# Kernel optimization log

Hardware: AMD Instinct MI355X
Metric: run time of the kernel (lower is better)

The kernel has to match this reference:

```python
import jax, jax.numpy as jnp
import numpy as np

V, H, B, S, T = 512, 1024, 128, 256, 128


def setup_inputs() -> dict:
    key = jax.random.key(0)
    ks = jax.random.split(key, 16)
    s = 1.0 / np.sqrt(H)
    f32 = jnp.float32
    return {
        "encoder_outputs": jax.random.normal(ks[0], (B, S, H), f32),
        "encoder_hidden": jax.random.normal(ks[1], (1, B, H), f32),
        "encoder_cell": jax.random.normal(ks[2], (1, B, H), f32),
        "target_tensor": jax.random.randint(ks[3], (B, T), 0, V),
        "max_length": T,
        "emb": (jax.random.normal(ks[4], (V, H), f32) * s),
        "Wa_w": jax.random.normal(ks[5], (H, H), f32) * s,
        "Wa_b": jnp.zeros((H,), f32),
        "Ua_w": jax.random.normal(ks[6], (H, H), f32) * s,
        "Ua_b": jnp.zeros((H,), f32),
        "Va_w": jax.random.normal(ks[7], (1, H), f32) * s,
        "Va_b": jnp.zeros((1,), f32),
        "W_ih": jax.random.normal(ks[8], (4 * H, 2 * H), f32) * s,
        "W_hh": jax.random.normal(ks[9], (4 * H, H), f32) * s,
        "b_ih": jnp.zeros((4 * H,), f32),
        "b_hh": jnp.zeros((4 * H,), f32),
        "out_w": jax.random.normal(ks[10], (V, H), f32) * s,
        "out_b": jnp.zeros((V,), f32),
    }


def reference(encoder_outputs, encoder_hidden, encoder_cell, target_tensor, max_length,
              emb, Wa_w, Wa_b, Ua_w, Ua_b, Va_w, Va_b,
              W_ih, W_hh, b_ih, b_hh, out_w, out_b):
    # Teacher forcing: decoder input at step i is SOS (=0) then target[:, i-1].
    bsz = encoder_outputs.shape[0]
    sos = jnp.zeros((bsz, 1), dtype=target_tensor.dtype)
    tokens = jnp.concatenate([sos, target_tensor[:, : max_length - 1]], axis=1)  # [B, T]
    xs = emb[tokens].transpose(1, 0, 2)  # [T, B, H] (dropout = identity, eval mode)

    # Ua(keys) is loop-invariant (original recomputes it each step; same math).
    keys_proj = jnp.einsum('bsh,kh->bsk', encoder_outputs, Ua_w) + Ua_b  # [B, S, H]

    def step(carry, emb_t):
        h, c = carry  # [B, H] each
        q = h @ Wa_w.T + Wa_b  # Bahdanau query projection [B, H]
        e = jnp.tanh(q[:, None, :] + keys_proj) @ Va_w[0] + Va_b[0]  # [B, S]
        w = jax.nn.softmax(e, axis=-1)
        ctx = jnp.einsum('bs,bsh->bh', w, encoder_outputs)
        x = jnp.concatenate([emb_t, ctx], axis=-1)  # [B, 2H]
        gates = x @ W_ih.T + b_ih + h @ W_hh.T + b_hh  # [B, 4H], torch order i,f,g,o
        i, f, g, o = jnp.split(gates, 4, axis=-1)
        c_new = jax.nn.sigmoid(f) * c + jax.nn.sigmoid(i) * jnp.tanh(g)
        h_new = jax.nn.sigmoid(o) * jnp.tanh(c_new)
        logits = h_new @ out_w.T + out_b  # [B, V]
        return (h_new, c_new), (logits, w)

    init = (encoder_hidden[0], encoder_cell[0])
    (h_fin, c_fin), (logits, attn) = jax.lax.scan(step, init, xs)
    log_probs = jax.nn.log_softmax(logits.transpose(1, 0, 2), axis=-1)  # [B, T, V]
    return log_probs, h_fin[None], attn.transpose(1, 0, 2)  # hidden [1,B,H], attn [B,T,S]
```

## Files before the change

kernel.cpp:

```cpp
#include <hip/hip_runtime.h>

#define B_ 128
#define S_ 256
#define H_ 1024
#define V_ 512
#define T_ 128
#define G4 4096

typedef __attribute__((ext_vector_type(8))) short bf16x8;
typedef __attribute__((ext_vector_type(4))) float f32x4;

__device__ __forceinline__ float bf2f(unsigned short x) {
    unsigned int u = ((unsigned int)x) << 16;
    return __builtin_bit_cast(float, u);
}
__device__ __forceinline__ unsigned short f2b(float f) {
    unsigned int u = __builtin_bit_cast(unsigned int, f);
    u = u + 0x7fffu + ((u >> 16) & 1u);
    return (unsigned short)(u >> 16);
}
__device__ __forceinline__ float ftanh(float x) {
    float e = __expf(2.f * x);
    return 1.f - 2.f * __builtin_amdgcn_rcpf(e + 1.f);
}
__device__ __forceinline__ float fsigm(float x) {
    return __builtin_amdgcn_rcpf(1.f + __expf(-x));
}
__device__ __forceinline__ void gll16(const void* g, void* l) {
    __builtin_amdgcn_global_load_lds(
        (const __attribute__((address_space(1))) unsigned int*)g,
        (__attribute__((address_space(3))) unsigned int*)l, 16, 0, 0);
}

__global__ void f32_to_bf16_x4(const float4* __restrict__ in, ushort4* __restrict__ out, int n4) {
    int i = blockIdx.x * 256 + threadIdx.x;
    if (i < n4) {
        float4 v = in[i];
        ushort4 o;
        o.x = f2b(v.x); o.y = f2b(v.y); o.z = f2b(v.z); o.w = f2b(v.w);
        out[i] = o;
    }
}

__global__ void cvt_gather(const float* __restrict__ src, int src_ld, int coff,
                           unsigned short* __restrict__ dst, int perm) {
    int i = blockIdx.x * 256 + threadIdx.x;
    int r = i >> 8;
    int c = (i & 255) * 4;
    int sr = perm ? (((r & 3) << 10) + (r >> 2)) : r;
    float4 v = *reinterpret_cast<const float4*>(src + (size_t)sr * src_ld + coff + c);
    ushort4 o;
    o.x = f2b(v.x); o.y = f2b(v.y); o.z = f2b(v.z); o.w = f2b(v.w);
    *reinterpret_cast<ushort4*>(dst + (size_t)r * 1024 + c) = o;
}

__global__ void build_toks(const int* __restrict__ target, int* __restrict__ toks) {
    int idx = blockIdx.x * 256 + threadIdx.x;
    if (idx < T_ * B_) {
        int t = idx / B_, b = idx % B_;
        toks[idx] = (t == 0) ? 0 : target[b * T_ + t - 1];
    }
}

__global__ void build_bsum(const float* __restrict__ b_ih, const float* __restrict__ b_hh,
                           float* __restrict__ bsum) {
    int j = blockIdx.x * 256 + threadIdx.x;
    if (j < G4) {
        int pj = ((j & 3) << 10) + (j >> 2);
        bsum[j] = b_ih[pj] + b_hh[pj];
    }
}

template<int MODE>
__global__ __launch_bounds__(256) void gemm_mf(
    const unsigned short* __restrict__ A,
    const unsigned short* __restrict__ Bw,
    int K, int ldb, int ldc,
    float* __restrict__ C, unsigned short* __restrict__ Cb,
    const float* __restrict__ bias)
{
    __shared__ unsigned short As[2 * 8192];
    __shared__ unsigned short Bs[2 * 8192];
    const int tid = threadIdx.x;
    const int lane = tid & 63;
    const int wv = tid >> 6;
    const int m0 = blockIdx.x * 64;
    const int n0 = blockIdx.y * 64;

    const unsigned short* ga[4];
    const unsigned short* gb[4];
    #pragma unroll
    for (int j = 0; j < 4; ++j) {
        int ci = tid + 256 * j;
        int row = ci >> 4;
        int src = (ci & 15) ^ (row & 7);
        ga[j] = A + (size_t)(m0 + row) * K + src * 8;
        gb[j] = Bw + (size_t)(n0 + row) * ldb + src * 8;
    }

    f32x4 acc[2][2] = {};
    const int r0 = (wv >> 1) * 32;
    const int cq0 = (wv & 1) * 32;
    const int fr = lane & 15;
    const int kg = lane >> 4;

    auto stage = [&](int k0, int p) {
        #pragma unroll
        for (int j = 0; j < 4; ++j) {
            gll16(ga[j] + k0, As + p * 8192 + j * 2048 + wv * 512);
            gll16(gb[j] + k0, Bs + p * 8192 + j * 2048 + wv * 512);
        }
    };

    stage(0, 0);
    stage(128, 1);
    int p = 0;
    for (int k0 = 0; k0 < K; k0 += 128) {
        if (k0 + 128 < K) {
            asm volatile("s_waitcnt vmcnt(8)" ::: "memory");
        } else {
            asm volatile("s_waitcnt vmcnt(0)" ::: "memory");
        }
        __builtin_amdgcn_sched_barrier(0);
        __builtin_amdgcn_s_barrier();
        __builtin_amdgcn_sched_barrier(0);
        const unsigned short* Ab = As + p * 8192;
        const unsigned short* Bb = Bs + p * 8192;
        bf16x8 af[2][4], bfr[2][4];
        #pragma unroll
        for (int f = 0; f < 2; ++f)
            #pragma unroll
            for (int kh = 0; kh < 4; ++kh) {
                int ra = r0 + f * 16 + fr;
                af[f][kh] = *(const bf16x8*)&Ab[ra * 128 + (((kh * 4 + kg) ^ (ra & 7)) << 3)];
                int rb = cq0 + f * 16 + fr;
                bfr[f][kh] = *(const bf16x8*)&Bb[rb * 128 + (((kh * 4 + kg) ^ (rb & 7)) << 3)];
            }
        asm volatile("s_waitcnt lgkmcnt(0)" ::: "memory");
        __builtin_amdgcn_sched_barrier(0);
        __builtin_amdgcn_s_barrier();
        __builtin_amdgcn_sched_barrier(0);
        if (k0 + 256 < K) stage(k0 + 256, p);
        #pragma unroll
        for (int f = 0; f < 2; ++f)
            #pragma unroll
            for (int g = 0; g < 2; ++g)
                #pragma unroll
                for (int kh = 0; kh < 4; ++kh)
                    acc[f][g] = __builtin_amdgcn_mfma_f32_16x16x32_bf16(
                        af[f][kh], bfr[g][kh], acc[f][g], 0, 0, 0);
        p ^= 1;
    }

    const int erow = (lane >> 4) * 4;
    const int ecol = lane & 15;
    #pragma unroll
    for (int f = 0; f < 2; ++f) {
        #pragma unroll
        for (int g = 0; g < 2; ++g) {
            #pragma unroll
            for (int r = 0; r < 4; ++r) {
                int row = m0 + r0 + f * 16 + erow + r;
                int col = n0 + cq0 + g * 16 + ecol;
                float v = acc[f][g][r] + bias[col];
                if (MODE == 0) C[(size_t)row * ldc + col] = v;
                else Cb[(size_t)row * ldc + col] = f2b(v);
            }
        }
    }
}

template<int MODE>
__global__ __launch_bounds__(256) void gemm_n32(
    const unsigned short* __restrict__ A,
    const unsigned short* __restrict__ Bw,
    int K, int ldb, int ldc,
    float* __restrict__ C, unsigned short* __restrict__ Cb,
    const float* __restrict__ bias,
    const float* __restrict__ Pemb,
    const int* __restrict__ toks,
    float* __restrict__ Cq,
    float* __restrict__ Lg,
    const float* __restrict__ bias2,
    int flag)
{
    __shared__ unsigned short As[2 * 8192];
    __shared__ unsigned short Bs[2 * 4096];
    const int tid = threadIdx.x;
    const int lane = tid & 63;
    const int wv = tid >> 6;
    const int m0 = blockIdx.x * 64;
    const int n0 = blockIdx.y * 32;

    const unsigned short* ga[4];
    const unsigned short* gb[2];
    #pragma unroll
    for (int j = 0; j < 4; ++j) {
        int ci = tid + 256 * j;
        int row = ci >> 4;
        int src = (ci & 15) ^ (row & 7);
        ga[j] = A + (size_t)(m0 + row) * K + src * 8;
    }
    #pragma unroll
    for (int j = 0; j < 2; ++j) {
        int ci = tid + 256 * j;
        int row = ci >> 4;
        int src = (ci & 15) ^ (row & 7);
        gb[j] = Bw + (size_t)(n0 + row) * ldb + src * 8;
    }

    f32x4 acc[2] = {};
    const int r0 = (wv >> 1) * 32;
    const int c0 = (wv & 1) * 16;
    const int fr = lane & 15;
    const int kg = lane >> 4;

    auto stage = [&](int k0, int p) {
        #pragma unroll
        for (int j = 0; j < 4; ++j)
            gll16(ga[j] + k0, As + p * 8192 + j * 2048 + wv * 512);
        #pragma unroll
        for (int j = 0; j < 2; ++j)
            gll16(gb[j] + k0, Bs + p * 4096 + j * 2048 + wv * 512);
    };

    stage(0, 0);
    stage(128, 1);
    int p = 0;
    for (int k0 = 0; k0 < K; k0 += 128) {
        if (k0 + 128 < K) {
            asm volatile("s_waitcnt vmcnt(6)" ::: "memory");
        } else {
            asm volatile("s_waitcnt vmcnt(0)" ::: "memory");
        }
        __builtin_amdgcn_sched_barrier(0);
        __builtin_amdgcn_s_barrier();
        __builtin_amdgcn_sched_barrier(0);
        const unsigned short* Ab = As + p * 8192;
        const unsigned short* Bb = Bs + p * 4096;
        bf16x8 af[2][4], bfr[4];
        #pragma unroll
        for (int kh = 0; kh < 4; ++kh) {
            #pragma unroll
            for (int f = 0; f < 2; ++f) {
                int ra = r0 + f * 16 + fr;
                af[f][kh] = *(const bf16x8*)&Ab[ra * 128 + (((kh * 4 + kg) ^ (ra & 7)) << 3)];
            }
            int rb = c0 + fr;
            bfr[kh] = *(const bf16x8*)&Bb[rb * 128 + (((kh * 4 + kg) ^ (rb & 7)) << 3)];
        }
        asm volatile("s_waitcnt lgkmcnt(0)" ::: "memory");
        __builtin_amdgcn_sched_barrier(0);
        __builtin_amdgcn_s_barrier();
        __builtin_amdgcn_sched_barrier(0);
        if (k0 + 256 < K) stage(k0 + 256, p);
        #pragma unroll
        for (int f = 0; f < 2; ++f)
            #pragma unroll
            for (int kh = 0; kh < 4; ++kh)
                acc[f] = __builtin_amdgcn_mfma_f32_16x16x32_bf16(
                    af[f][kh], bfr[kh], acc[f], 0, 0, 0);
        p ^= 1;
    }

    const int erow = (lane >> 4) * 4;
    const int ecol = lane & 15;

    if constexpr (MODE == 4) {
        __shared__ float Lt[64 * 32];
        __syncthreads();
        #pragma unroll
        for (int f = 0; f < 2; ++f)
            #pragma unroll
            for (int r = 0; r < 4; ++r)
                Lt[(r0 + f * 16 + erow + r) * 32 + c0 + ecol] = acc[f][r];
        __syncthreads();
        #pragma unroll
        for (int i = 0; i < 2; ++i) {
            int pi = tid + 256 * i;
            int r = pi >> 3, u = pi & 7;
            int b = m0 + r;
            int hh = (n0 >> 2) + u;
            f32x4 gv = *reinterpret_cast<const f32x4*>(&Lt[r * 32 + u * 4]);
            const float* gp = C + (size_t)b * G4 + n0 + u * 4;
            float iv = gv[0] + gp[0];
            float fv = gv[1] + gp[1];
            float gg = gv[2] + gp[2];
            float ov = gv[3] + gp[3];
            int ci = b * H_ + hh;
            float cn = fsigm(fv) * Cq[ci] + fsigm(iv) * ftanh(gg);
            float hn = fsigm(ov) * ftanh(cn);
            Cq[ci] = cn;
            Cb[ci] = f2b(hn);
            if (flag) Lg[ci] = hn;
        }
    } else {
        #pragma unroll
        for (int f = 0; f < 2; ++f) {
            #pragma unroll
            for (int r = 0; r < 4; ++r) {
                int row = m0 + r0 + f * 16 + erow + r;
                int col = n0 + c0 + ecol;
                float v = acc[f][r];
                if (MODE == 0) {
                    C[(size_t)row * ldc + col] = v + bias[col];
                } else {
                    if (col < H_) {
                        Cq[(size_t)row * H_ + col] = v + bias[col];
                    } else if (col < 5120) {
                        int cg = col - H_;
                        C[(size_t)row * G4 + cg] = v + Pemb[(size_t)toks[row] * G4 + cg];
                    } else {
                        int cl = col - 5120;
                        Lg[(size_t)row * V_ + cl] = v + bias2[cl];
                    }
                }
            }
        }
    }
}

__global__ __launch_bounds__(256) void attn_e(
    const unsigned short* __restrict__ kp,
    const float* __restrict__ q,
    const float* __restrict__ Va,
    const unsigned short* __restrict__ encb,
    float* __restrict__ es_g,
    float* __restrict__ pctx,
    const float* __restrict__ lg,
    float* __restrict__ lp,
    int t)
{
    const int b = blockIdx.x;
    const int sh = blockIdx.y;
    const int tid = threadIdx.x;
    const int lane = tid & 63;
    const int wv = tid >> 6;
    __shared__ float qs[H_];
    __shared__ float vas[H_];
    __shared__ float es[16], pe[16];
    __shared__ float redm[4], reds[4];

    *reinterpret_cast<float4*>(&qs[tid * 4]) =
        *reinterpret_cast<const float4*>(&q[(size_t)b * H_ + tid * 4]);
    *reinterpret_cast<float4*>(&vas[tid * 4]) =
        *reinterpret_cast<const float4*>(&Va[tid * 4]);

    const bool doL = (t > 0) && (sh == 0);
    float a0 = doL ? lg[(size_t)b * V_ + tid] : -3.4e38f;
    float a1 = doL ? lg[(size_t)b * V_ + 256 + tid] : -3.4e38f;
    float mx = fmaxf(a0, a1);
    #pragma unroll
    for (int off = 32; off; off >>= 1) mx = fmaxf(mx, __shfl_xor(mx, off));
    if (lane == 0) redm[wv] = mx;
    __syncthreads();
    mx = fmaxf(fmaxf(redm[0], redm[1]), fmaxf(redm[2], redm[3]));
    float sm = doL ? (__expf(a0 - mx) + __expf(a1 - mx)) : 0.f;
    #pragma unroll
    for (int off = 32; off; off >>= 1) sm += __shfl_xor(sm, off);
    if (lane == 0) reds[wv] = sm;
    __syncthreads();
    if (doL) {
        sm = reds[0] + reds[1] + reds[2] + reds[3];
        float lse = mx + __logf(sm);
        size_t off = ((size_t)b * T_ + (t - 1)) * V_;
        lp[off + tid] = a0 - lse;
        lp[off + tid + 256] = a1 - lse;
    }

    #pragma unroll
    for (int si = 0; si < 4; ++si) {
        int s_loc = wv * 4 + si;
        const unsigned short* kr = kp + (size_t)(b * S_ + sh * 16 + s_loc) * H_;
        float acc = 0.f;
        #pragma unroll
        for (int it = 0; it < 4; ++it) {
            int h4 = lane * 4 + it * 256;
            ushort4 u = *reinterpret_cast<const ushort4*>(kr + h4);
            acc += vas[h4 + 0] * ftanh(qs[h4 + 0] + bf2f(u.x));
            acc += vas[h4 + 1] * ftanh(qs[h4 + 1] + bf2f(u.y));
            acc += vas[h4 + 2] * ftanh(qs[h4 + 2] + bf2f(u.z));
            acc += vas[h4 + 3] * ftanh(qs[h4 + 3] + bf2f(u.w));
        }
        #pragma unroll
        for (int off = 32; off; off >>= 1) acc += __shfl_down(acc, off);
        if (lane == 0) {
            es[s_loc] = acc;
            es_g[(size_t)b * S_ + sh * 16 + s_loc] = acc;
        }
    }
    __syncthreads();

    float mb = es[0];
    #pragma unroll
    for (int i = 1; i < 16; ++i) mb = fmaxf(mb, es[i]);
    if (tid < 16) pe[tid] = __expf(es[tid] - mb);
    __syncthreads();
    const int c0 = tid * 4;
    float ax = 0.f, ay = 0.f, az = 0.f, aw = 0.f;
    #pragma unroll
    for (int sl = 0; sl < 16; ++sl) {
        ushort4 u = *reinterpret_cast<const ushort4*>(
            &encb[(size_t)(b * S_ + sh * 16 + sl) * H_ + c0]);
        float w = pe[sl];
        ax += w * bf2f(u.x);
        ay += w * bf2f(u.y);
        az += w * bf2f(u.z);
        aw += w * bf2f(u.w);
    }
    float4 o4; o4.x = ax; o4.y = ay; o4.z = az; o4.w = aw;
    *reinterpret_cast<float4*>(&pctx[((size_t)b * 16 + sh) * H_ + c0]) = o4;
}

__global__ __launch_bounds__(256) void attn_comb(
    const float* __restrict__ es_g,
    const float* __restrict__ pctx,
    unsigned short* __restrict__ ctxb,
    float* __restrict__ attnOut,
    int t)
{
    const int b = blockIdx.x;
    const int tid = threadIdx.x;
    const int lane = tid & 63;
    const int wv = tid >> 6;
    __shared__ float es[S_], sc[16];
    __shared__ float redm[4], reds[4];

    float x = es_g[(size_t)b * S_ + tid];
    es[tid] = x;
    float mx = x;
    #pragma unroll
    for (int off = 32; off; off >>= 1) mx = fmaxf(mx, __shfl_xor(mx, off));
    if (lane == 0) redm[wv] = mx;
    __syncthreads();
    mx = fmaxf(fmaxf(redm[0], redm[1]), fmaxf(redm[2], redm[3]));
    float ex = __expf(x - mx);
    float sm = ex;
    #pragma unroll
    for (int off = 32; off; off >>= 1) sm += __shfl_xor(sm, off);
    if (lane == 0) reds[wv] = sm;
    __syncthreads();
    sm = reds[0] + reds[1] + reds[2] + reds[3];
    float rZ = __builtin_amdgcn_rcpf(sm);
    attnOut[((size_t)(b * T_ + t)) * S_ + tid] = ex * rZ;
    if (tid < 16) {
        float mb = es[tid * 16];
        #pragma unroll
        for (int j = 1; j < 16; ++j) mb = fmaxf(mb, es[tid * 16 + j]);
        sc[tid] = __expf(mb - mx);
    }
    __syncthreads();
    const int c0 = tid * 4;
    float ax = 0.f, ay = 0.f, az = 0.f, aw = 0.f;
    #pragma unroll
    for (int blk = 0; blk < 16; ++blk) {
        float4 pv = *reinterpret_cast<const float4*>(
            &pctx[((size_t)b * 16 + blk) * H_ + c0]);
        float s = sc[blk];
        ax += s * pv.x; ay += s * pv.y; az += s * pv.z; aw += s * pv.w;
    }
    ushort4 o;
    o.x = f2b(ax * rZ); o.y = f2b(ay * rZ); o.z = f2b(az * rZ); o.w = f2b(aw * rZ);
    *reinterpret_cast<ushort4*>(&ctxb[(size_t)b * H_ + c0]) = o;
}

__global__ __launch_bounds__(256) void lsm_kernel(
    const float* __restrict__ lg, float* __restrict__ lp, int t)
{
    int b = blockIdx.x, tid = threadIdx.x;
    int lane = tid & 63, wv = tid >> 6;
    __shared__ float red[4];
    float a0 = lg[(size_t)b * V_ + tid];
    float a1 = lg[(size_t)b * V_ + 256 + tid];
    float mx = fmaxf(a0, a1);
    #pragma unroll
    for (int off = 32; off; off >>= 1) mx = fmaxf(mx, __shfl_xor(mx, off));
    if (lane == 0) red[wv] = mx;
    __syncthreads();
    mx = fmaxf(fmaxf(red[0], red[1]), fmaxf(red[2], red[3]));
    float sm = __expf(a0 - mx) + __expf(a1 - mx);
    #pragma unroll
    for (int off = 32; off; off >>= 1) sm += __shfl_xor(sm, off);
    __syncthreads();
    if (lane == 0) red[wv] = sm;
    __syncthreads();
    sm = red[0] + red[1] + red[2] + red[3];
    float lse = mx + __logf(sm);
    size_t off = ((size_t)b * T_ + t) * V_;
    lp[off + tid] = a0 - lse;
    lp[off + tid + 256] = a1 - lse;
}

extern "C" void kernel_launch(void* const* d_in, const int* in_sizes, int n_in,
                              void* d_out, int out_size, void* d_ws, size_t ws_size,
                              hipStream_t stream) {
    const float* enc   = (const float*)d_in[0];
    const float* h0    = (const float*)d_in[1];
    const float* c0    = (const float*)d_in[2];
    const int*   targ  = (const int*)d_in[3];
    const float* emb   = (const float*)d_in[5];
    const float* Wa_w  = (const float*)d_in[6];
    const float* Wa_b  = (const float*)d_in[7];
    const float* Ua_w  = (const float*)d_in[8];
    const float* Ua_b  = (const float*)d_in[9];
    const float* Va_w  = (const float*)d_in[10];
    const float* W_ih  = (const float*)d_in[12];
    const float* W_hh  = (const float*)d_in[13];
    const float* b_ih  = (const float*)d_in[14];
    const float* b_hh  = (const float*)d_in[15];
    const float* out_w = (const float*)d_in[16];
    const float* out_b = (const float*)d_in[17];

    float* out  = (float*)d_out;
    float* lp   = out;
    float* hid  = out + (size_t)B_ * T_ * V_;
    float* attn = hid + (size_t)B_ * H_;

    char* w = (char*)d_ws;
    auto alloc = [&](size_t bytes) {
        char* p = w;
        w += (bytes + 255) & ~(size_t)255;
        return p;
    };
    const size_t NKP = (size_t)B_ * S_ * H_;
    unsigned short* kp     = (unsigned short*)alloc(NKP * 2);
    unsigned short* encb   = (unsigned short*)alloc(NKP * 2);
    unsigned short* Wcat_b = (unsigned short*)alloc((size_t)5632 * H_ * 2);
    unsigned short* Wih1_b = (unsigned short*)alloc((size_t)G4 * H_ * 2);
    unsigned short* Wih2_b = (unsigned short*)alloc((size_t)G4 * H_ * 2);
    unsigned short* Uaw_b  = (unsigned short*)alloc((size_t)H_ * H_ * 2);
    unsigned short* emb_b  = (unsigned short*)alloc((size_t)V_ * H_ * 2);
    unsigned short* hb     = (unsigned short*)alloc((size_t)B_ * H_ * 2);
    unsigned short* ctxb   = (unsigned short*)alloc((size_t)B_ * H_ * 2);
    float* Pemb  = (float*)alloc((size_t)V_ * G4 * 4);
    float* bsumP = (float*)alloc((size_t)G4 * 4);
    int*   toks  = (int*)alloc((size_t)T_ * B_ * 4);
    float* cbuf  = (float*)alloc((size_t)B_ * H_ * 4);
    float* qbuf  = (float*)alloc((size_t)B_ * H_ * 4);
    float* gates = (float*)alloc((size_t)B_ * G4 * 4);
    float* lgbuf = (float*)alloc((size_t)B_ * V_ * 4);
    float* es_g  = (float*)alloc((size_t)B_ * S_ * 4);
    float* pctx  = (float*)alloc((size_t)B_ * 16 * H_ * 4);
    if ((size_t)(w - (char*)d_ws) > ws_size) return;

    auto cvt = [&](const float* src, unsigned short* dst, size_t n) {
        int n4 = (int)(n / 4);
        f32_to_bf16_x4<<<(n4 + 255) / 256, 256, 0, stream>>>((const float4*)src, (ushort4*)dst, n4);
    };

    cvt(enc, encb, NKP);
    cvt(Ua_w, Uaw_b, (size_t)H_ * H_);
    cvt(emb, emb_b, (size_t)V_ * H_);
    cvt(h0, hb, (size_t)B_ * H_);
    cvt_gather<<<1024, 256, 0, stream>>>(Wa_w, H_, 0, Wcat_b, 0);
    cvt_gather<<<4096, 256, 0, stream>>>(W_hh, H_, 0, Wcat_b + (size_t)1024 * H_, 1);
    cvt_gather<<<512, 256, 0, stream>>>(out_w, H_, 0, Wcat_b + (size_t)5120 * H_, 0);
    cvt_gather<<<4096, 256, 0, stream>>>(W_ih, 2 * H_, 0, Wih1_b, 1);
    cvt_gather<<<4096, 256, 0, stream>>>(W_ih, 2 * H_, H_, Wih2_b, 1);
    build_toks<<<(T_ * B_ + 255) / 256, 256, 0, stream>>>(targ, toks);
    build_bsum<<<(G4 + 255) / 256, 256, 0, stream>>>(b_ih, b_hh, bsumP);
    hipMemcpyAsync(cbuf, c0, (size_t)B_ * H_ * 4, hipMemcpyDeviceToDevice, stream);

    gemm_mf<1><<<dim3((B_ * S_) / 64, H_ / 64), 256, 0, stream>>>(
        encb, Uaw_b, H_, H_, H_, nullptr, kp, Ua_b);
    gemm_mf<0><<<dim3(V_ / 64, G4 / 64), 256, 0, stream>>>(
        emb_b, Wih1_b, H_, H_, G4, Pemb, nullptr, bsumP);

    for (int t = 0; t < T_; ++t) {
        gemm_n32<2><<<dim3(2, 176), 256, 0, stream>>>(
            hb, Wcat_b, H_, H_, 0, gates, nullptr, Wa_b,
            Pemb, toks + t * B_, qbuf, lgbuf, out_b, 0);
        attn_e<<<dim3(B_, 16), 256, 0, stream>>>(
            kp, qbuf, Va_w, encb, es_g, pctx, lgbuf, lp, t);
        attn_comb<<<B_, 256, 0, stream>>>(es_g, pctx, ctxb, attn, t);
        gemm_n32<4><<<dim3(2, 128), 256, 0, stream>>>(
            ctxb, Wih2_b, H_, H_, 0, gates, hb, nullptr,
            nullptr, nullptr, cbuf, hid, nullptr, t == T_ - 1);
    }
    gemm_n32<0><<<dim3(2, 16), 256, 0, stream>>>(
        hb, Wcat_b + (size_t)5120 * H_, H_, H_, V_, lgbuf, nullptr, out_b,
        nullptr, nullptr, nullptr, nullptr, nullptr, 0);
    lsm_kernel<<<B_, 256, 0, stream>>>(lgbuf, lp, T_ - 1);
}
```

Before: 6.317 ms.

## Drop max-subtraction in attention softmax, split combine over H, raise MFMA wave priority

```diff
diff --git a/kernel.cpp b/kernel.cpp
--- a/kernel.cpp
+++ b/kernel.cpp
@@ -141,6 +141,7 @@
         __builtin_amdgcn_s_barrier();
         __builtin_amdgcn_sched_barrier(0);
         if (k0 + 256 < K) stage(k0 + 256, p);
+        __builtin_amdgcn_s_setprio(1);
         #pragma unroll
         for (int f = 0; f < 2; ++f)
             #pragma unroll
@@ -149,6 +150,7 @@
                 for (int kh = 0; kh < 4; ++kh)
                     acc[f][g] = __builtin_amdgcn_mfma_f32_16x16x32_bf16(
                         af[f][kh], bfr[g][kh], acc[f][g], 0, 0, 0);
+        __builtin_amdgcn_s_setprio(0);
         p ^= 1;
     }
 
@@ -254,12 +256,14 @@
         __builtin_amdgcn_s_barrier();
         __builtin_amdgcn_sched_barrier(0);
         if (k0 + 256 < K) stage(k0 + 256, p);
+        __builtin_amdgcn_s_setprio(1);
         #pragma unroll
         for (int f = 0; f < 2; ++f)
             #pragma unroll
             for (int kh = 0; kh < 4; ++kh)
                 acc[f] = __builtin_amdgcn_mfma_f32_16x16x32_bf16(
                     af[f][kh], bfr[kh], acc[f], 0, 0, 0);
+        __builtin_amdgcn_s_setprio(0);
         p ^= 1;
     }
 
@@ -338,7 +342,7 @@
     const int wv = tid >> 6;
     __shared__ float qs[H_];
     __shared__ float vas[H_];
-    __shared__ float es[16], pe[16];
+    __shared__ float pe[16];
     __shared__ float redm[4], reds[4];
 
     *reinterpret_cast<float4*>(&qs[tid * 4]) =
@@ -385,17 +389,12 @@
         #pragma unroll
         for (int off = 32; off; off >>= 1) acc += __shfl_down(acc, off);
         if (lane == 0) {
-            es[s_loc] = acc;
+            pe[s_loc] = __expf(acc);
             es_g[(size_t)b * S_ + sh * 16 + s_loc] = acc;
         }
     }
     __syncthreads();
 
-    float mb = es[0];
-    #pragma unroll
-    for (int i = 1; i < 16; ++i) mb = fmaxf(mb, es[i]);
-    if (tid < 16) pe[tid] = __expf(es[tid] - mb);
-    __syncthreads();
     const int c0 = tid * 4;
     float ax = 0.f, ay = 0.f, az = 0.f, aw = 0.f;
     #pragma unroll
@@ -420,21 +419,13 @@
     int t)
 {
     const int b = blockIdx.x;
+    const int hh = blockIdx.y;
     const int tid = threadIdx.x;
     const int lane = tid & 63;
     const int wv = tid >> 6;
-    __shared__ float es[S_], sc[16];
-    __shared__ float redm[4], reds[4];
-
-    float x = es_g[(size_t)b * S_ + tid];
-    es[tid] = x;
-    float mx = x;
-    #pragma unroll
-    for (int off = 32; off; off >>= 1) mx = fmaxf(mx, __shfl_xor(mx, off));
-    if (lane == 0) redm[wv] = mx;
-    __syncthreads();
-    mx = fmaxf(fmaxf(redm[0], redm[1]), fmaxf(redm[2], redm[3]));
-    float ex = __expf(x - mx);
+    __shared__ float reds[4];
+
+    float ex = __expf(es_g[(size_t)b * S_ + tid]);
     float sm = ex;
     #pragma unroll
     for (int off = 32; off; off >>= 1) sm += __shfl_xor(sm, off);
@@ -442,26 +433,18 @@
     __syncthreads();
     sm = reds[0] + reds[1] + reds[2] + reds[3];
     float rZ = __builtin_amdgcn_rcpf(sm);
-    attnOut[((size_t)(b * T_ + t)) * S_ + tid] = ex * rZ;
-    if (tid < 16) {
-        float mb = es[tid * 16];
-        #pragma unroll
-        for (int j = 1; j < 16; ++j) mb = fmaxf(mb, es[tid * 16 + j]);
-        sc[tid] = __expf(mb - mx);
-    }
-    __syncthreads();
-    const int c0 = tid * 4;
-    float ax = 0.f, ay = 0.f, az = 0.f, aw = 0.f;
+    if (hh == 0) attnOut[((size_t)(b * T_ + t)) * S_ + tid] = ex * rZ;
+
+    const int c0 = hh * 512 + tid * 2;
+    float a0 = 0.f, a1 = 0.f;
     #pragma unroll
     for (int blk = 0; blk < 16; ++blk) {
-        float4 pv = *reinterpret_cast<const float4*>(
+        float2 pv = *reinterpret_cast<const float2*>(
             &pctx[((size_t)b * 16 + blk) * H_ + c0]);
-        float s = sc[blk];
-        ax += s * pv.x; ay += s * pv.y; az += s * pv.z; aw += s * pv.w;
-    }
-    ushort4 o;
-    o.x = f2b(ax * rZ); o.y = f2b(ay * rZ); o.z = f2b(az * rZ); o.w = f2b(aw * rZ);
-    *reinterpret_cast<ushort4*>(&ctxb[(size_t)b * H_ + c0]) = o;
+        a0 += pv.x; a1 += pv.y;
+    }
+    ushort2 o; o.x = f2b(a0 * rZ); o.y = f2b(a1 * rZ);
+    *reinterpret_cast<ushort2*>(&ctxb[(size_t)b * H_ + c0]) = o;
 }
 
 __global__ __launch_bounds__(256) void lsm_kernel(
@@ -572,7 +555,7 @@
             Pemb, toks + t * B_, qbuf, lgbuf, out_b, 0);
         attn_e<<<dim3(B_, 16), 256, 0, stream>>>(
             kp, qbuf, Va_w, encb, es_g, pctx, lgbuf, lp, t);
-        attn_comb<<<B_, 256, 0, stream>>>(es_g, pctx, ctxb, attn, t);
+        attn_comb<<<dim3(B_, 2), 256, 0, stream>>>(es_g, pctx, ctxb, attn, t);
         gemm_n32<4><<<dim3(2, 128), 256, 0, stream>>>(
             ctxb, Wih2_b, H_, H_, 0, gates, hb, nullptr,
             nullptr, nullptr, cbuf, hid, nullptr, t == T_ - 1);
```

After: 6.266 ms. No clear change (-0.8%).
